# Performance work log

Measured on AMD Instinct MI355X. Metric: run time of the kernel, lower is better.

## Reference

```python
import jax, jax.numpy as jnp
import numpy as np


def setup_inputs() -> dict:
    key = jax.random.key(0)
    ks = jax.random.split(key, 8)
    B, T, I, H, O = 4096, 2048, 4, 20, 4
    s_ih = 1.0 / np.sqrt(H)
    return {
        "x": jax.random.normal(ks[0], (B, T, I), dtype=jnp.float32),
        "h0": jax.random.normal(ks[1], (B, H), dtype=jnp.float32),
        "W_ih": jax.random.uniform(ks[2], (H, I), jnp.float32, -s_ih, s_ih),
        "W_hh": jax.random.uniform(ks[3], (H, H), jnp.float32, -s_ih, s_ih),
        "b_ih": jax.random.uniform(ks[4], (H,), jnp.float32, -s_ih, s_ih),
        "b_hh": jax.random.uniform(ks[5], (H,), jnp.float32, -s_ih, s_ih),
        "fc_w": jax.random.uniform(ks[6], (O, H), jnp.float32, -s_ih, s_ih),
        "fc_b": jax.random.uniform(ks[7], (O,), jnp.float32, -s_ih, s_ih),
    }


def reference(x, h0, W_ih, W_hh, b_ih, b_hh, fc_w, fc_b):
    # x: [B, T, I] batch_first; vanilla tanh RNN recurrence.
    # Precompute the input projection for all timesteps in one GEMM.
    xi = jnp.einsum("bti,hi->tbh", x, W_ih) + b_ih + b_hh  # [T, B, H]

    def step(h, xt):
        h = jnp.tanh(xt + h @ W_hh.T)  # [B, H]
        return h, None

    h_last, _ = jax.lax.scan(step, h0, xi)
    # Module takes last timestep only, then Linear(H -> 4).
    return h_last @ fc_w.T + fc_b  # [B, 4]
```

## Files before the change

kernel.cpp:

```cpp
#include <hip/hip_runtime.h>
#include <cstddef>


typedef float f32x2 __attribute__((ext_vector_type(2)));
typedef float f32x4 __attribute__((ext_vector_type(4)));

constexpr int Tn   = 2048;
constexpr int Hn   = 20;
constexpr int EPB  = 16;
constexpr int SB   = 16;
constexpr int NBLK = Tn / SB;

__global__ __launch_bounds__(256, 1) void rnn_fwd(
    const float* __restrict__ x,
    const float* __restrict__ h0,
    const float* __restrict__ W_ih,
    const float* __restrict__ W_hh,
    const float* __restrict__ b_ih,
    const float* __restrict__ b_hh,
    const float* __restrict__ fc_w,
    const float* __restrict__ fc_b,
    float* __restrict__ out)
{
    __shared__ __align__(16) f32x4 xlds[2][EPB][SB + 1];
    __shared__ float hsh[EPB][24];

    const int tid  = threadIdx.x;
    const int j    = tid & 15;
    const int e    = tid >> 4;
    const int b    = blockIdx.x * EPB + e;
    const int uB   = 16 + (j & 3);
    const int lane = tid & 63;

    const int i12 = (((lane & ~15) | ((lane - 12) & 15))) << 2;
    const int i13 = (((lane & ~15) | ((lane - 13) & 15))) << 2;
    const int i14 = (((lane & ~15) | ((lane - 14) & 15))) << 2;
    const int i15 = (((lane & ~15) | ((lane - 15) & 15))) << 2;

    const float S = 2.88539008177792681472f;

    f32x2 w2[16];
#pragma unroll
    for (int r = 0; r < 16; ++r) {
        const int k = (j - r) & 15;
        w2[r] = f32x2{S * W_hh[j * Hn + k], S * W_hh[uB * Hn + k]};
    }
    f32x2 wqr[4], xiw[4];
#pragma unroll
    for (int c = 0; c < 4; ++c) {
        const int qc = 16 + ((j + c) & 3);
        wqr[c] = f32x2{S * W_hh[j * Hn + qc], S * W_hh[uB * Hn + qc]};
        xiw[c] = f32x2{S * W_ih[j * 4 + c],  S * W_ih[uB * 4 + c]};
    }
    f32x2 bias2 = f32x2{S * (b_ih[j] + b_hh[j]), S * (b_ih[uB] + b_hh[uB])};

    float rA = 0.5f * (1.0f - h0[b * Hn + j]);
    float rB = 0.5f * (1.0f - h0[b * Hn + uB]);

    const f32x4* __restrict__ xp =
        reinterpret_cast<const f32x4*>(x) + (size_t)b * Tn;

#define DPPM " row_mask:0xf bank_mask:0xf\n\t"
#define PKB  " op_sel:[0,0,0] op_sel_hi:[1,0,1]\n\t"
#define CLB  "v40","v41","v42","v43","v44","v45","v46","v47","v48","v49",     \
             "v50","v51","v52","v53","v54","v55","v56","v57","v58","v59",     \
             "v60","v61","v62","v63"

#define STEP_MAC() do {                                                       \
    asm volatile(                                                             \
  "v_fma_f32 v44, %[rB], -2.0, 1.0\n\t"                 \
  "v_fma_f32 v40, %[rA], -2.0, 1.0\n\t"                 \
  "ds_bpermute_b32 v50, %[i12], v40\n\t"                                      \
  "ds_bpermute_b32 v52, %[i13], v40\n\t"                                      \
  "ds_bpermute_b32 v54, %[i14], v40\n\t"                                      \
  "ds_bpermute_b32 v56, %[i15], v40\n\t"                                      \
  "v_pk_fma_f32 %[P], %[w0], v[40:41], %[P]" PKB              \
  "v_mov_b32_dpp v42, v44 quad_perm:[1,2,3,0]" DPPM                           \
  "v_pk_fma_f32 %[Q], %[c0], v[44:45], %[Q]" PKB             \
  "v_mov_b32_dpp v46, v44 quad_perm:[2,3,0,1]" DPPM                           \
  "v_pk_fma_f32 %[P], %[c1], v[42:43], %[P]" PKB                              \
  "v_mov_b32_dpp v48, v44 quad_perm:[3,0,1,2]" DPPM                           \
  "v_pk_fma_f32 %[Q], %[c2], v[46:47], %[Q]" PKB                              \
  "v_mov_b32_dpp v42, v40 row_ror:1"  DPPM                                    \
  "v_pk_fma_f32 %[P], %[c3], v[48:49], %[P]" PKB                              \
  "v_mov_b32_dpp v46, v40 row_ror:2"  DPPM                                    \
  "v_pk_fma_f32 %[Q], %[w1], v[42:43], %[Q]" PKB                              \
  "v_mov_b32_dpp v48, v40 row_ror:3"  DPPM                                    \
  "v_pk_fma_f32 %[P], %[w2], v[46:47], %[P]" PKB                              \
  "v_mov_b32_dpp v42, v40 row_ror:4"  DPPM                                    \
  "v_pk_fma_f32 %[Q], %[w3], v[48:49], %[Q]" PKB                              \
  "v_mov_b32_dpp v46, v40 row_ror:5"  DPPM                                    \
  "v_pk_fma_f32 %[P], %[w4], v[42:43], %[P]" PKB                              \
  "v_mov_b32_dpp v48, v40 row_ror:6"  DPPM                                    \
  "v_pk_fma_f32 %[Q], %[w5], v[46:47], %[Q]" PKB                              \
  "v_mov_b32_dpp v42, v40 row_ror:7"  DPPM                                    \
  "v_pk_fma_f32 %[P], %[w6], v[48:49], %[P]" PKB                              \
  "v_mov_b32_dpp v46, v40 row_ror:8"  DPPM                                    \
  "v_pk_fma_f32 %[Q], %[w7], v[42:43], %[Q]" PKB                              \
  "v_mov_b32_dpp v48, v40 row_ror:9"  DPPM                                    \
  "v_pk_fma_f32 %[P], %[w8], v[46:47], %[P]" PKB                              \
  "v_mov_b32_dpp v42, v40 row_ror:10" DPPM                                    \
  "v_pk_fma_f32 %[Q], %[w9], v[48:49], %[Q]" PKB                              \
  "v_mov_b32_dpp v46, v40 row_ror:11" DPPM                                    \
  "v_pk_fma_f32 %[P], %[w10], v[42:43], %[P]" PKB                             \
  "v_pk_fma_f32 %[Q], %[w11], v[46:47], %[Q]"                                 \
  " op_sel:[0,0,0] op_sel_hi:[1,0,1]"                                         \
  : [P] "+v"(xiP), [Q] "+v"(xiQ)                                              \
  : [rA] "v"(rA), [rB] "v"(rB),                                               \
    [w0] "v"(w2[0]), [w1] "v"(w2[1]),  [w2] "v"(w2[2]),  [w3] "v"(w2[3]),     \
    [w4] "v"(w2[4]), [w5] "v"(w2[5]),  [w6] "v"(w2[6]),  [w7] "v"(w2[7]),     \
    [w8] "v"(w2[8]), [w9] "v"(w2[9]),  [w10] "v"(w2[10]),[w11] "v"(w2[11]),   \
    [c0] "v"(wqr[0]), [c1] "v"(wqr[1]), [c2] "v"(wqr[2]), [c3] "v"(wqr[3]),   \
    [i12] "v"(i12), [i13] "v"(i13), [i14] "v"(i14), [i15] "v"(i15)            \
  : CLB, "memory");                                                           \
} while (0)

#define STEP_TAIL(XV) do {                                                    \
    f32x2 xa_ = __builtin_shufflevector((XV), (XV), 0, 1);                    \
    f32x2 xb_ = __builtin_shufflevector((XV), (XV), 2, 3);                    \
    asm volatile(                                                             \
  "s_waitcnt lgkmcnt(0)\n\t"                                                  \
  "v_pk_fma_f32 %[P], %[w12], v[50:51], %[P]" PKB                   \
  "v_pk_fma_f32 %[Q], %[w13], v[52:53], %[Q]" PKB                   \
  "v_pk_fma_f32 %[P], %[w14], v[54:55], %[P]" PKB                   \
  "v_pk_fma_f32 %[Q], %[w15], v[56:57], %[Q]" PKB                   \
  "v_pk_add_f32 v[58:59], %[P], %[Q]\n\t"                                     \
  "v_pk_fma_f32 %[P], %[x0], %[xa], %[b2]" PKB                                \
  "v_pk_mul_f32 %[Q], %[x1], %[xa] op_sel:[0,1] op_sel_hi:[1,1]\n\t"          \
  "v_exp_f32 v60, v59\n\t"                                                    \
  "v_pk_fma_f32 %[P], %[x2], %[xb], %[P]" PKB                                 \
  "v_exp_f32 v61, v58\n\t"                                                    \
  "v_pk_fma_f32 %[Q], %[x3], %[xb], %[Q] op_sel:[0,1,0] op_sel_hi:[1,1,1]\n\t"\
  "v_add_f32 v60, 1.0, v60\n\t"                                               \
  "v_add_f32 v61, 1.0, v61\n\t"                                               \
  "v_rcp_f32 %[rB], v60\n\t"                                                  \
  "v_rcp_f32 %[rA], v61"                                                      \
  : [rA] "=&v"(rA), [rB] "=&v"(rB),                                           \
    [P] "+v"(xiP), [Q] "+v"(xiQ)                                              \
  : [w12] "v"(w2[12]), [w13] "v"(w2[13]), [w14] "v"(w2[14]), [w15] "v"(w2[15]),\
    [xa] "v"(xa_), [xb] "v"(xb_),                                             \
    [x0] "v"(xiw[0]), [x1] "v"(xiw[1]), [x2] "v"(xiw[2]), [x3] "v"(xiw[3]),   \
    [b2] "v"(bias2)                                                           \
  : CLB, "memory");                                                           \
} while (0)

#define STEP(XV) do { STEP_MAC(); STEP_TAIL(XV); } while (0)

    xlds[0][e][j] = xp[j];
    f32x4 x0v = xp[0];
    f32x2 xiP, xiQ;
    xiP[0] = __builtin_fmaf(x0v[2], xiw[2][0],
             __builtin_fmaf(x0v[0], xiw[0][0], bias2[0]));
    xiP[1] = __builtin_fmaf(x0v[2], xiw[2][1],
             __builtin_fmaf(x0v[0], xiw[0][1], bias2[1]));
    xiQ[0] = __builtin_fmaf(x0v[3], xiw[3][0], x0v[1] * xiw[1][0]);
    xiQ[1] = __builtin_fmaf(x0v[3], xiw[3][1], x0v[1] * xiw[1][1]);
    f32x4 q0 = xlds[0][e][1];
    f32x4 q1 = xlds[0][e][2];
    f32x4 q2 = xlds[0][e][3];

    int cur = 0;
#pragma unroll 1
    for (int k = 0; k < NBLK; ++k) {
        const int kn = (k + 1 < NBLK) ? (k + 1) : (NBLK - 1);
        f32x4 xr = xp[kn * SB + j];
        const int nxt = cur ^ 1;
#pragma unroll
        for (int s = 0; s < SB - 4; ++s) {
            f32x4 xv = q0; q0 = q1; q1 = q2;
            q2 = xlds[cur][e][s + 4];
            STEP(xv);
        }
        xlds[nxt][e][j] = xr;
        { f32x4 xv = q0; q0 = q1; q1 = q2; q2 = xlds[nxt][e][0]; STEP(xv); }
        { f32x4 xv = q0; q0 = q1; q1 = q2; q2 = xlds[nxt][e][1]; STEP(xv); }
        { f32x4 xv = q0; q0 = q1; q1 = q2; q2 = xlds[nxt][e][2]; STEP(xv); }
        { f32x4 xv = q0; q0 = q1; q1 = q2; q2 = xlds[nxt][e][3]; STEP(xv); }
        cur = nxt;
    }
#undef STEP
#undef STEP_MAC
#undef STEP_TAIL
#undef PKB
#undef DPPM
#undef CLB

    const float hAf = __builtin_fmaf(-2.0f, rA, 1.0f);
    const float hBf = __builtin_fmaf(-2.0f, rB, 1.0f);

    hsh[e][j] = hAf;
    if (j < 4) hsh[e][16 + j] = hBf;
    if (j < 4) {
        float o = fc_b[j];
#pragma unroll
        for (int kk = 0; kk < Hn; ++kk)
            o = __builtin_fmaf(hsh[e][kk], fc_w[j * Hn + kk], o);
        out[b * 4 + j] = o;
    }
}

extern "C" void kernel_launch(void* const* d_in, const int* in_sizes, int n_in,
                              void* d_out, int out_size, void* d_ws, size_t ws_size,
                              hipStream_t stream) {
    const float* x    = (const float*)d_in[0];
    const float* h0   = (const float*)d_in[1];
    const float* W_ih = (const float*)d_in[2];
    const float* W_hh = (const float*)d_in[3];
    const float* b_ih = (const float*)d_in[4];
    const float* b_hh = (const float*)d_in[5];
    const float* fc_w = (const float*)d_in[6];
    const float* fc_b = (const float*)d_in[7];
    float* out = (float*)d_out;

    rnn_fwd<<<dim3(256), dim3(256), 0, stream>>>(x, h0, W_ih, W_hh, b_ih, b_hh,
                                                 fc_w, fc_b, out);
}
```

Baseline: 425.0 us.

## Fold tanh affine into weights and replace bpermute with full DPP rotations

Rewrites h = 1-2r by folding the -2 factor into W_hh and the row sums of W_hh into the bias, so each step works directly on the reciprocal r with no per-step conversion FMAs. The four ds_bpermute LDS shuffles and their lgkmcnt wait are replaced by DPP row_ror 12-15 moves, taking LDS off the serial recurrence's critical path. The recurrent state now lives in hardcoded v40/v44 across separate asm blocks with no compiler-visible dependency, which is fragile if the compiler allocates those registers between the asm blocks.

```diff
diff --git a/kernel.cpp b/kernel.cpp
--- a/kernel.cpp
+++ b/kernel.cpp
@@ -25,37 +25,39 @@
     __shared__ __align__(16) f32x4 xlds[2][EPB][SB + 1];
     __shared__ float hsh[EPB][24];
 
-    const int tid  = threadIdx.x;
-    const int j    = tid & 15;
-    const int e    = tid >> 4;
-    const int b    = blockIdx.x * EPB + e;
-    const int uB   = 16 + (j & 3);
-    const int lane = tid & 63;
-
-    const int i12 = (((lane & ~15) | ((lane - 12) & 15))) << 2;
-    const int i13 = (((lane & ~15) | ((lane - 13) & 15))) << 2;
-    const int i14 = (((lane & ~15) | ((lane - 14) & 15))) << 2;
-    const int i15 = (((lane & ~15) | ((lane - 15) & 15))) << 2;
+    const int tid = threadIdx.x;
+    const int j   = tid & 15;
+    const int e   = tid >> 4;
+    const int b   = blockIdx.x * EPB + e;
+    const int uB  = 16 + (j & 3);
 
     const float S = 2.88539008177792681472f;
+    const float M = -2.0f * S;
 
     f32x2 w2[16];
 #pragma unroll
     for (int r = 0; r < 16; ++r) {
         const int k = (j - r) & 15;
-        w2[r] = f32x2{S * W_hh[j * Hn + k], S * W_hh[uB * Hn + k]};
+        w2[r] = f32x2{M * W_hh[j * Hn + k], M * W_hh[uB * Hn + k]};
     }
     f32x2 wqr[4], xiw[4];
 #pragma unroll
     for (int c = 0; c < 4; ++c) {
         const int qc = 16 + ((j + c) & 3);
-        wqr[c] = f32x2{S * W_hh[j * Hn + qc], S * W_hh[uB * Hn + qc]};
+        wqr[c] = f32x2{M * W_hh[j * Hn + qc], M * W_hh[uB * Hn + qc]};
         xiw[c] = f32x2{S * W_ih[j * 4 + c],  S * W_ih[uB * 4 + c]};
     }
-    f32x2 bias2 = f32x2{S * (b_ih[j] + b_hh[j]), S * (b_ih[uB] + b_hh[uB])};
-
-    float rA = 0.5f * (1.0f - h0[b * Hn + j]);
-    float rB = 0.5f * (1.0f - h0[b * Hn + uB]);
+    float rsA = 0.0f, rsB = 0.0f;
+#pragma unroll
+    for (int k = 0; k < Hn; ++k) {
+        rsA += W_hh[j  * Hn + k];
+        rsB += W_hh[uB * Hn + k];
+    }
+    f32x2 bias2 = f32x2{S * (b_ih[j]  + b_hh[j]  + rsA),
+                        S * (b_ih[uB] + b_hh[uB] + rsB)};
+
+    const float r0A = 0.5f * (1.0f - h0[b * Hn + j]);
+    const float r0B = 0.5f * (1.0f - h0[b * Hn + uB]);
 
     const f32x4* __restrict__ xp =
         reinterpret_cast<const f32x4*>(x) + (size_t)b * Tn;
@@ -63,85 +65,78 @@
 #define DPPM " row_mask:0xf bank_mask:0xf\n\t"
 #define PKB  " op_sel:[0,0,0] op_sel_hi:[1,0,1]\n\t"
 #define CLB  "v40","v41","v42","v43","v44","v45","v46","v47","v48","v49",     \
-             "v50","v51","v52","v53","v54","v55","v56","v57","v58","v59",     \
-             "v60","v61","v62","v63"
+             "v50","v51","v52","v53"
 
 #define STEP_MAC() do {                                                       \
     asm volatile(                                                             \
-  "v_fma_f32 v44, %[rB], -2.0, 1.0\n\t"                 \
-  "v_fma_f32 v40, %[rA], -2.0, 1.0\n\t"                 \
-  "ds_bpermute_b32 v50, %[i12], v40\n\t"                                      \
-  "ds_bpermute_b32 v52, %[i13], v40\n\t"                                      \
-  "ds_bpermute_b32 v54, %[i14], v40\n\t"                                      \
-  "ds_bpermute_b32 v56, %[i15], v40\n\t"                                      \
+  "v_pk_fma_f32 %[Q], %[c0], v[44:45], %[Q]" PKB             \
+  "v_mov_b32_dpp v42, v44 quad_perm:[1,2,3,0]" DPPM                           \
   "v_pk_fma_f32 %[P], %[w0], v[40:41], %[P]" PKB              \
-  "v_mov_b32_dpp v42, v44 quad_perm:[1,2,3,0]" DPPM                           \
-  "v_pk_fma_f32 %[Q], %[c0], v[44:45], %[Q]" PKB             \
   "v_mov_b32_dpp v46, v44 quad_perm:[2,3,0,1]" DPPM                           \
-  "v_pk_fma_f32 %[P], %[c1], v[42:43], %[P]" PKB                              \
+  "v_pk_fma_f32 %[Q], %[c1], v[42:43], %[Q]" PKB                              \
   "v_mov_b32_dpp v48, v44 quad_perm:[3,0,1,2]" DPPM                           \
-  "v_pk_fma_f32 %[Q], %[c2], v[46:47], %[Q]" PKB                              \
+  "v_pk_fma_f32 %[P], %[c2], v[46:47], %[P]" PKB                              \
   "v_mov_b32_dpp v42, v40 row_ror:1"  DPPM                                    \
-  "v_pk_fma_f32 %[P], %[c3], v[48:49], %[P]" PKB                              \
+  "v_pk_fma_f32 %[Q], %[c3], v[48:49], %[Q]" PKB                              \
   "v_mov_b32_dpp v46, v40 row_ror:2"  DPPM                                    \
-  "v_pk_fma_f32 %[Q], %[w1], v[42:43], %[Q]" PKB                              \
+  "v_pk_fma_f32 %[P], %[w1], v[42:43], %[P]" PKB                              \
   "v_mov_b32_dpp v48, v40 row_ror:3"  DPPM                                    \
-  "v_pk_fma_f32 %[P], %[w2], v[46:47], %[P]" PKB                              \
+  "v_pk_fma_f32 %[Q], %[w2], v[46:47], %[Q]" PKB                              \
   "v_mov_b32_dpp v42, v40 row_ror:4"  DPPM                                    \
-  "v_pk_fma_f32 %[Q], %[w3], v[48:49], %[Q]" PKB                              \
+  "v_pk_fma_f32 %[P], %[w3], v[48:49], %[P]" PKB                              \
   "v_mov_b32_dpp v46, v40 row_ror:5"  DPPM                                    \
-  "v_pk_fma_f32 %[P], %[w4], v[42:43], %[P]" PKB                              \
+  "v_pk_fma_f32 %[Q], %[w4], v[42:43], %[Q]" PKB                              \
   "v_mov_b32_dpp v48, v40 row_ror:6"  DPPM                                    \
-  "v_pk_fma_f32 %[Q], %[w5], v[46:47], %[Q]" PKB                              \
+  "v_pk_fma_f32 %[P], %[w5], v[46:47], %[P]" PKB                              \
   "v_mov_b32_dpp v42, v40 row_ror:7"  DPPM                                    \
-  "v_pk_fma_f32 %[P], %[w6], v[48:49], %[P]" PKB                              \
+  "v_pk_fma_f32 %[Q], %[w6], v[48:49], %[Q]" PKB                              \
   "v_mov_b32_dpp v46, v40 row_ror:8"  DPPM                                    \
-  "v_pk_fma_f32 %[Q], %[w7], v[42:43], %[Q]" PKB                              \
+  "v_pk_fma_f32 %[P], %[w7], v[42:43], %[P]" PKB                              \
   "v_mov_b32_dpp v48, v40 row_ror:9"  DPPM                                    \
-  "v_pk_fma_f32 %[P], %[w8], v[46:47], %[P]" PKB                              \
+  "v_pk_fma_f32 %[Q], %[w8], v[46:47], %[Q]" PKB                              \
   "v_mov_b32_dpp v42, v40 row_ror:10" DPPM                                    \
-  "v_pk_fma_f32 %[Q], %[w9], v[48:49], %[Q]" PKB                              \
+  "v_pk_fma_f32 %[P], %[w9], v[48:49], %[P]" PKB                              \
   "v_mov_b32_dpp v46, v40 row_ror:11" DPPM                                    \
-  "v_pk_fma_f32 %[P], %[w10], v[42:43], %[P]" PKB                             \
-  "v_pk_fma_f32 %[Q], %[w11], v[46:47], %[Q]"                                 \
+  "v_pk_fma_f32 %[Q], %[w10], v[42:43], %[Q]" PKB                             \
+  "v_mov_b32_dpp v48, v40 row_ror:12" DPPM                                    \
+  "v_pk_fma_f32 %[P], %[w11], v[46:47], %[P]" PKB                             \
+  "v_mov_b32_dpp v42, v40 row_ror:13" DPPM                                    \
+  "v_pk_fma_f32 %[Q], %[w12], v[48:49], %[Q]" PKB                             \
+  "v_mov_b32_dpp v46, v40 row_ror:14" DPPM                                    \
+  "v_pk_fma_f32 %[P], %[w13], v[42:43], %[P]" PKB                             \
+  "v_mov_b32_dpp v48, v40 row_ror:15" DPPM                                    \
+  "v_pk_fma_f32 %[Q], %[w14], v[46:47], %[Q]" PKB                             \
+  "v_pk_fma_f32 %[P], %[w15], v[48:49], %[P]"                                 \
   " op_sel:[0,0,0] op_sel_hi:[1,0,1]"                                         \
   : [P] "+v"(xiP), [Q] "+v"(xiQ)                                              \
-  : [rA] "v"(rA), [rB] "v"(rB),                                               \
-    [w0] "v"(w2[0]), [w1] "v"(w2[1]),  [w2] "v"(w2[2]),  [w3] "v"(w2[3]),     \
+  : [w0] "v"(w2[0]), [w1] "v"(w2[1]),  [w2] "v"(w2[2]),  [w3] "v"(w2[3]),     \
     [w4] "v"(w2[4]), [w5] "v"(w2[5]),  [w6] "v"(w2[6]),  [w7] "v"(w2[7]),     \
     [w8] "v"(w2[8]), [w9] "v"(w2[9]),  [w10] "v"(w2[10]),[w11] "v"(w2[11]),   \
-    [c0] "v"(wqr[0]), [c1] "v"(wqr[1]), [c2] "v"(wqr[2]), [c3] "v"(wqr[3]),   \
-    [i12] "v"(i12), [i13] "v"(i13), [i14] "v"(i14), [i15] "v"(i15)            \
-  : CLB, "memory");                                                           \
+    [w12] "v"(w2[12]),[w13] "v"(w2[13]),[w14] "v"(w2[14]),[w15] "v"(w2[15]),  \
+    [c0] "v"(wqr[0]), [c1] "v"(wqr[1]), [c2] "v"(wqr[2]), [c3] "v"(wqr[3])    \
+  : CLB);                                                                     \
 } while (0)
 
 #define STEP_TAIL(XV) do {                                                    \
     f32x2 xa_ = __builtin_shufflevector((XV), (XV), 0, 1);                    \
     f32x2 xb_ = __builtin_shufflevector((XV), (XV), 2, 3);                    \
     asm volatile(                                                             \
-  "s_waitcnt lgkmcnt(0)\n\t"                                                  \
-  "v_pk_fma_f32 %[P], %[w12], v[50:51], %[P]" PKB                   \
-  "v_pk_fma_f32 %[Q], %[w13], v[52:53], %[Q]" PKB                   \
-  "v_pk_fma_f32 %[P], %[w14], v[54:55], %[P]" PKB                   \
-  "v_pk_fma_f32 %[Q], %[w15], v[56:57], %[Q]" PKB                   \
-  "v_pk_add_f32 v[58:59], %[P], %[Q]\n\t"                                     \
+  "v_pk_add_f32 v[50:51], %[P], %[Q]\n\t"                                     \
   "v_pk_fma_f32 %[P], %[x0], %[xa], %[b2]" PKB                                \
   "v_pk_mul_f32 %[Q], %[x1], %[xa] op_sel:[0,1] op_sel_hi:[1,1]\n\t"          \
-  "v_exp_f32 v60, v59\n\t"                                                    \
+  "v_exp_f32 v52, v51\n\t"                                                    \
   "v_pk_fma_f32 %[P], %[x2], %[xb], %[P]" PKB                                 \
-  "v_exp_f32 v61, v58\n\t"                                                    \
+  "v_exp_f32 v53, v50\n\t"                                                    \
   "v_pk_fma_f32 %[Q], %[x3], %[xb], %[Q] op_sel:[0,1,0] op_sel_hi:[1,1,1]\n\t"\
-  "v_add_f32 v60, 1.0, v60\n\t"                                               \
-  "v_add_f32 v61, 1.0, v61\n\t"                                               \
-  "v_rcp_f32 %[rB], v60\n\t"                                                  \
-  "v_rcp_f32 %[rA], v61"                                                      \
-  : [rA] "=&v"(rA), [rB] "=&v"(rB),                                           \
-    [P] "+v"(xiP), [Q] "+v"(xiQ)                                              \
-  : [w12] "v"(w2[12]), [w13] "v"(w2[13]), [w14] "v"(w2[14]), [w15] "v"(w2[15]),\
-    [xa] "v"(xa_), [xb] "v"(xb_),                                             \
+  "v_add_f32 v52, 1.0, v52\n\t"                                               \
+  "v_add_f32 v53, 1.0, v53\n\t"                                               \
+  "v_rcp_f32 v44, v52\n\t"                                                    \
+  "v_rcp_f32 v40, v53"                                                        \
+  : [P] "+v"(xiP), [Q] "+v"(xiQ)                                              \
+  : [xa] "v"(xa_), [xb] "v"(xb_),                                             \
     [x0] "v"(xiw[0]), [x1] "v"(xiw[1]), [x2] "v"(xiw[2]), [x3] "v"(xiw[3]),   \
     [b2] "v"(bias2)                                                           \
-  : CLB, "memory");                                                           \
+  : CLB);                                                                     \
 } while (0)
 
 #define STEP(XV) do { STEP_MAC(); STEP_TAIL(XV); } while (0)
@@ -155,6 +150,8 @@
              __builtin_fmaf(x0v[0], xiw[0][1], bias2[1]));
     xiQ[0] = __builtin_fmaf(x0v[3], xiw[3][0], x0v[1] * xiw[1][0]);
     xiQ[1] = __builtin_fmaf(x0v[3], xiw[3][1], x0v[1] * xiw[1][1]);
+    asm volatile("v_mov_b32 v40, %0\n\tv_mov_b32 v44, %1"
+                 :: "v"(r0A), "v"(r0B) : "v40", "v44");
     f32x4 q0 = xlds[0][e][1];
     f32x4 q1 = xlds[0][e][2];
     f32x4 q2 = xlds[0][e][3];
@@ -185,8 +182,11 @@
 #undef DPPM
 #undef CLB
 
-    const float hAf = __builtin_fmaf(-2.0f, rA, 1.0f);
-    const float hBf = __builtin_fmaf(-2.0f, rB, 1.0f);
+    float rAf, rBf;
+    asm volatile("v_mov_b32 %0, v40\n\tv_mov_b32 %1, v44"
+                 : "=v"(rAf), "=v"(rBf));
+    const float hAf = __builtin_fmaf(-2.0f, rAf, 1.0f);
+    const float hBf = __builtin_fmaf(-2.0f, rBf, 1.0f);
 
     hsh[e][j] = hAf;
     if (j < 4) hsh[e][16 + j] = hBf;
```

Result: faster. 380.8 us (-10.4%).
